# Optimization experiments

Measured on AMD Instinct MI355X. Metric: run time of the kernel, lower is better.

Reference implementation:

```python
import jax, jax.numpy as jnp
import numpy as np

N_NODES = 50000
N_EDGES = 800000
DIM = 256


def setup_inputs() -> dict:
    key = jax.random.key(0)
    k1, k2, k3, k4 = jax.random.split(key, 4)
    x = jax.random.normal(k1, (N_NODES, DIM), dtype=jnp.float32)
    edge_index = jax.random.randint(k2, (2, N_EDGES), 0, N_NODES, dtype=jnp.int64)
    # GCNConv learned params (glorot-style weight, zero bias like PyG default init)
    W = jax.random.normal(k3, (DIM, DIM), dtype=jnp.float32) * (1.0 / np.sqrt(DIM))
    b = jnp.zeros((DIM,), dtype=jnp.float32)
    return {"x": x, "edge_index": edge_index, "W": W, "b": b}


def reference(x, edge_index, W, b):
    # GNNBlock forward (eval mode: dropout is identity; normalizer=Identity,
    # activation=ReLU, projection=Identity since in_dim==out_dim).
    n = x.shape[0]
    # --- GCNConv with self-loops and symmetric normalization ---
    loop = jnp.arange(n, dtype=edge_index.dtype)
    src = jnp.concatenate([edge_index[0], loop])  # [E+N]
    dst = jnp.concatenate([edge_index[1], loop])  # [E+N]
    ones = jnp.ones(src.shape[0], dtype=x.dtype)
    deg = jax.ops.segment_sum(ones, dst, num_segments=n)  # in-degree incl. self-loop
    dinv = jnp.where(deg > 0, jax.lax.rsqrt(deg), 0.0)
    norm = dinv[src] * dinv[dst]  # [E+N]
    h = x @ W  # transform first (in->out), then aggregate
    msg = h[src] * norm[:, None]  # gather + scale, [E+N, DIM]
    agg = jax.ops.segment_sum(msg, dst, num_segments=n) + b  # scatter-add
    # --- norm (Identity) -> activation (ReLU) -> residual -> dropout (eval) ---
    out = jax.nn.relu(agg) + x
    return out
```

## Files before the change

### kernel.cpp

```cpp
#include <hip/hip_runtime.h>

#define N_NODES 50000
#define DIM 256
#define NBUCK 196
#define BCAP 6144
#define CEDGES 2048
#define APAD 264
#define EPAD 260
#define TROWS 32

typedef __attribute__((ext_vector_type(8))) short bf16x8;
typedef __attribute__((ext_vector_type(4))) float f32x4;
typedef __attribute__((ext_vector_type(2))) float f32x2;
union U16 { uint4 u; bf16x8 s; };

__device__ __forceinline__ unsigned short f2b(float f) {
    unsigned int u = __float_as_uint(f);
    return (unsigned short)((u + 0x7FFFu + ((u >> 16) & 1u)) >> 16);
}

__global__ __launch_bounds__(256) void prep_bin_kernel(const int* __restrict__ src,
                                                       const int* __restrict__ dst, int E,
                                                       int nCoarse,
                                                       unsigned int* __restrict__ slab2,
                                                       int* __restrict__ meta,
                                                       const float* __restrict__ W,
                                                       uint4* __restrict__ Bpack,
                                                       const float* __restrict__ x,
                                                       unsigned int* __restrict__ xq) {
    __shared__ int hist[NBUCK];
    __shared__ int scn[NBUCK];
    __shared__ int cur[NBUCK];
    __shared__ int s2[256];
    __shared__ unsigned int sorted[CEDGES];

    const int tid = threadIdx.x;

    if (blockIdx.x >= (unsigned)nCoarse) {
        int role = blockIdx.x - nCoarse;
        if (role < 32) {
            int gid  = role * 256 + tid;
            int lane = gid & 63;
            int u    = (gid >> 6) & 15;
            int ki   = gid >> 10;
            int n    = u * 16 + (lane & 15);
            int k0   = ki * 32 + (lane >> 4) * 8;
            unsigned int w[4];
            #pragma unroll
            for (int p = 0; p < 4; ++p) {
                unsigned int lo = f2b(W[(size_t)(k0 + 2 * p) * DIM + n]);
                unsigned int hi = f2b(W[(size_t)(k0 + 2 * p + 1) * DIM + n]);
                w[p] = lo | (hi << 16);
            }
            Bpack[gid] = make_uint4(w[0], w[1], w[2], w[3]);
        } else {
            int gid = (role - 32) * 256 + tid;
            float4 v = ((const float4*)x)[gid];
            int p = __builtin_amdgcn_cvt_pk_fp8_f32(v.x, v.y, 0, false);
            p     = __builtin_amdgcn_cvt_pk_fp8_f32(v.z, v.w, p, true);
            xq[gid] = (unsigned int)p;
        }
        return;
    }

    const int e0 = blockIdx.x * CEDGES;
    const int nE = min(CEDGES, E - e0);

    if (tid < NBUCK) hist[tid] = 0;
    __syncthreads();

    unsigned int pk[8];
    #pragma unroll
    for (int i = 0; i < 8; ++i) {
        int idx = i * 256 + tid;
        pk[i] = 0xFFFFFFFFu;
        if (idx < nE) {
            unsigned int s = (unsigned int)src[e0 + idx];
            unsigned int d = (unsigned int)dst[e0 + idx];
            pk[i] = (d << 16) | s;
            atomicAdd(&hist[d >> 8], 1);
        }
    }
    __syncthreads();

    int v = (tid < NBUCK) ? hist[tid] : 0;
    s2[tid] = v;
    __syncthreads();
    for (int off = 1; off < 256; off <<= 1) {
        int t = (tid >= off) ? s2[tid - off] : 0;
        __syncthreads();
        s2[tid] += t;
        __syncthreads();
    }
    if (tid < NBUCK) {
        scn[tid] = s2[tid] - v;
        cur[tid] = 0;
    }
    __syncthreads();

    #pragma unroll
    for (int i = 0; i < 8; ++i) {
        if (pk[i] != 0xFFFFFFFFu) {
            int bkt = pk[i] >> 24;
            int p = scn[bkt] + atomicAdd(&cur[bkt], 1);
            sorted[p] = pk[i];
        }
    }
    __syncthreads();

    for (int i = tid; i < nE; i += 256)
        slab2[(size_t)blockIdx.x * CEDGES + i] = sorted[i];
    if (tid < NBUCK)
        meta[blockIdx.x * NBUCK + tid] = (scn[tid] << 16) | (hist[tid] & 0xFFFF);
}

__global__ __launch_bounds__(256) void fine_kernel(int nCoarse,
                                                   const unsigned int* __restrict__ slab2,
                                                   const int* __restrict__ meta,
                                                   int* __restrict__ offs,
                                                   int* __restrict__ deg,
                                                   float* __restrict__ dinv,
                                                   int* __restrict__ csr_src) {
    __shared__ int hist[256];
    __shared__ int scn[256];
    __shared__ unsigned int stage[BCAP];
    __shared__ int lcur;

    const int tid = threadIdx.x;
    const int g = blockIdx.x;

    if (tid == 0) lcur = 0;
    hist[tid] = 0;
    __syncthreads();

    for (int b = tid; b < nCoarse; b += 256) {
        int m = meta[b * NBUCK + g];
        int n  = m & 0xFFFF;
        int st = (m >> 16) & 0xFFFF;
        if (n > 0) {
            int pos = atomicAdd(&lcur, n);
            const unsigned int* rs = slab2 + (size_t)b * CEDGES + st;
            for (int k = 0; k < n; ++k) {
                if (pos + k < BCAP) {
                    unsigned int p = rs[k];
                    stage[pos + k] = p;
                    atomicAdd(&hist[(p >> 16) & 255], 1);
                }
            }
        }
    }
    __syncthreads();
    const int cnt = min(lcur, BCAP);

    int d = hist[tid];
    scn[tid] = d;
    __syncthreads();
    for (int off = 1; off < 256; off <<= 1) {
        int t = (tid >= off) ? scn[tid - off] : 0;
        __syncthreads();
        scn[tid] += t;
        __syncthreads();
    }
    int excl = scn[tid] - d;

    int node = g * 256 + tid;
    const int base = g * BCAP;
    if (node < N_NODES) {
        offs[node] = base + excl;
        deg[node]  = d;
        dinv[node] = rsqrtf((float)(d + 1));
    }
    hist[tid] = excl;
    __syncthreads();

    for (int i = tid; i < cnt; i += 256) {
        unsigned int p = stage[i];
        int pos = atomicAdd(&hist[(p >> 16) & 255], 1);
        csr_src[base + pos] = (int)(p & 0xFFFFu);
    }
}

__global__ __launch_bounds__(256) void agg_gemm_kernel(const unsigned int* __restrict__ xq,
                                                       const int* __restrict__ offs,
                                                       const int* __restrict__ deg,
                                                       const int* __restrict__ csr_src,
                                                       const float* __restrict__ dinv,
                                                       const float* __restrict__ x,
                                                       const uint4* __restrict__ Bpack,
                                                       const float* __restrict__ b,
                                                       float* __restrict__ out) {
    __shared__ __align__(16) char LDSraw[TROWS * EPAD * 4];
    ushort* ALDS = (ushort*)LDSraw;
    float*  ELDS = (float*)LDSraw;

    const int tid  = threadIdx.x;
    const int wave = tid >> 6;
    const int lane = tid & 63;
    const int row0 = blockIdx.x * TROWS;

    for (int j = 0; j < 8; ++j) {
        const int r   = wave * 8 + j;
        const int row = row0 + r;
        ushort4 st4 = make_ushort4(0, 0, 0, 0);
        if (row < N_NODES) {
            const float di = dinv[row];
            unsigned int qself = xq[(size_t)row * 64 + lane];
            f32x2 lo = __builtin_amdgcn_cvt_pk_f32_fp8((int)qself, false);
            f32x2 hi = __builtin_amdgcn_cvt_pk_f32_fp8((int)qself, true);
            float ax = lo.x * di, ay = lo.y * di, az = hi.x * di, aw = hi.y * di;

            const int start = offs[row];
            const int n     = deg[row];
            int i = 0;
            for (; i + 8 <= n; i += 8) {
                int s0 = csr_src[start + i + 0], s1 = csr_src[start + i + 1];
                int s2 = csr_src[start + i + 2], s3 = csr_src[start + i + 3];
                int s4 = csr_src[start + i + 4], s5 = csr_src[start + i + 5];
                int s6 = csr_src[start + i + 6], s7 = csr_src[start + i + 7];
                unsigned int q0 = xq[(size_t)s0 * 64 + lane];
                unsigned int q1 = xq[(size_t)s1 * 64 + lane];
                unsigned int q2 = xq[(size_t)s2 * 64 + lane];
                unsigned int q3 = xq[(size_t)s3 * 64 + lane];
                unsigned int q4 = xq[(size_t)s4 * 64 + lane];
                unsigned int q5 = xq[(size_t)s5 * 64 + lane];
                unsigned int q6 = xq[(size_t)s6 * 64 + lane];
                unsigned int q7 = xq[(size_t)s7 * 64 + lane];
                float d0 = dinv[s0], d1 = dinv[s1], d2 = dinv[s2], d3 = dinv[s3];
                float d4 = dinv[s4], d5 = dinv[s5], d6 = dinv[s6], d7 = dinv[s7];
                #pragma unroll
                for (int u = 0; u < 8; ++u) {
                    unsigned int q; float dd;
                    switch (u) {
                        case 0: q = q0; dd = d0; break; case 1: q = q1; dd = d1; break;
                        case 2: q = q2; dd = d2; break; case 3: q = q3; dd = d3; break;
                        case 4: q = q4; dd = d4; break; case 5: q = q5; dd = d5; break;
                        case 6: q = q6; dd = d6; break; default: q = q7; dd = d7; break;
                    }
                    f32x2 l = __builtin_amdgcn_cvt_pk_f32_fp8((int)q, false);
                    f32x2 h = __builtin_amdgcn_cvt_pk_f32_fp8((int)q, true);
                    ax += l.x * dd; ay += l.y * dd; az += h.x * dd; aw += h.y * dd;
                }
            }
            for (; i < n; ++i) {
                int s = csr_src[start + i];
                unsigned int q = xq[(size_t)s * 64 + lane];
                float dd = dinv[s];
                f32x2 l = __builtin_amdgcn_cvt_pk_f32_fp8((int)q, false);
                f32x2 h = __builtin_amdgcn_cvt_pk_f32_fp8((int)q, true);
                ax += l.x * dd; ay += l.y * dd; az += h.x * dd; aw += h.y * dd;
            }
            ax *= di; ay *= di; az *= di; aw *= di;
            st4 = make_ushort4(f2b(ax), f2b(ay), f2b(az), f2b(aw));
        }
        *(ushort4*)&ALDS[r * APAD + lane * 4] = st4;
    }
    __syncthreads();

    const int m  = lane & 15;
    const int kb = lane >> 4;

    f32x4 acc[2][4];
    #pragma unroll
    for (int r = 0; r < 2; ++r)
        #pragma unroll
        for (int t = 0; t < 4; ++t) acc[r][t] = (f32x4){0.f, 0.f, 0.f, 0.f};

    const uint4* bp = Bpack + (size_t)(wave * 4) * 64 + lane;

    for (int ki = 0; ki < 8; ++ki) {
        U16 bf[4], af[2];
        #pragma unroll
        for (int t = 0; t < 4; ++t) bf[t].u = bp[(size_t)(ki * 16 + t) * 64];
        #pragma unroll
        for (int r = 0; r < 2; ++r)
            af[r].u = *(const uint4*)&ALDS[(r * 16 + m) * APAD + ki * 32 + kb * 8];
        #pragma unroll
        for (int r = 0; r < 2; ++r)
            #pragma unroll
            for (int t = 0; t < 4; ++t)
                acc[r][t] = __builtin_amdgcn_mfma_f32_16x16x32_bf16(af[r].s, bf[t].s, acc[r][t], 0, 0, 0);
    }

    __syncthreads();
    #pragma unroll
    for (int t = 0; t < 4; ++t) {
        #pragma unroll
        for (int rl = 0; rl < 2; ++rl) {
            #pragma unroll
            for (int reg = 0; reg < 4; ++reg) {
                ELDS[(rl * 16 + kb * 4 + reg) * EPAD + wave * 64 + t * 16 + m] = acc[rl][t][reg];
            }
        }
    }
    __syncthreads();

    const float4* x4g = (const float4*)x;
    const float4* b4  = (const float4*)b;
    float4* out4 = (float4*)out;

    #pragma unroll
    for (int j = 0; j < 8; ++j) {
        int idx  = j * 256 + tid;
        int lrow = idx >> 6;
        int c4   = idx & 63;
        int grow = row0 + lrow;
        if (grow < N_NODES) {
            float4 v  = *(const float4*)&ELDS[lrow * EPAD + c4 * 4];
            float4 bb = b4[c4];
            float4 xx = x4g[(size_t)grow * 64 + c4];
            float4 o;
            o.x = fmaxf(v.x + bb.x, 0.f) + xx.x;
            o.y = fmaxf(v.y + bb.y, 0.f) + xx.y;
            o.z = fmaxf(v.z + bb.z, 0.f) + xx.z;
            o.w = fmaxf(v.w + bb.w, 0.f) + xx.w;
            out4[(size_t)grow * 64 + c4] = o;
        }
    }
}

extern "C" void kernel_launch(void* const* d_in, const int* in_sizes, int n_in,
                              void* d_out, int out_size, void* d_ws, size_t ws_size,
                              hipStream_t stream) {
    const float* x  = (const float*)d_in[0];
    const int*   ei = (const int*)d_in[1];
    const float* W  = (const float*)d_in[2];
    const float* b  = (const float*)d_in[3];
    float* out = (float*)d_out;
    const int E = in_sizes[1] / 2;

    char* ws = (char*)d_ws;
    int*          deg     = (int*)(ws);
    int*          offs    = (int*)(ws + 262144);
    float*        dinv    = (float*)(ws + 524288);
    int*          csr_src = (int*)(ws + 786432);
    int*          meta    = (int*)(ws + 5767168);
    unsigned int* slab2   = (unsigned int*)(ws + 6291456);
    uint4*        Bpack   = (uint4*)(ws + 9699328);
    unsigned int* xq      = (unsigned int*)(ws + 10485760);

    const int* src = ei;
    const int* dst = ei + E;

    const int nCoarse = (E + CEDGES - 1) / CEDGES;
    const int nXq = (N_NODES * 64) / 256;

    prep_bin_kernel<<<nCoarse + 32 + nXq, 256, 0, stream>>>(src, dst, E, nCoarse,
                                                            slab2, meta, W, Bpack, x, xq);
    fine_kernel<<<NBUCK, 256, 0, stream>>>(nCoarse, slab2, meta, offs, deg, dinv, csr_src);
    agg_gemm_kernel<<<(N_NODES + TROWS - 1) / TROWS, 256, 0, stream>>>(xq, offs, deg, csr_src,
                                                                       dinv, x, Bpack, b, out);
}
```

Baseline: 208.4 us.

## Parallelize fine-bucket gather via prefix-scanned run map; halve agg-GEMM tile rows

```diff
diff --git a/kernel.cpp b/kernel.cpp
--- a/kernel.cpp
+++ b/kernel.cpp
@@ -7,7 +7,7 @@
 #define CEDGES 2048
 #define APAD 264
 #define EPAD 260
-#define TROWS 32
+#define TROWS 16
 
 typedef __attribute__((ext_vector_type(8))) short bf16x8;
 typedef __attribute__((ext_vector_type(4))) float f32x4;
@@ -121,36 +121,61 @@
                                                    int* __restrict__ deg,
                                                    float* __restrict__ dinv,
                                                    int* __restrict__ csr_src) {
+    __shared__ int rcnt[512];
+    __shared__ int rst[512];
+    __shared__ int rbase[512];
+    __shared__ int scn[256];
     __shared__ int hist[256];
-    __shared__ int scn[256];
+    __shared__ unsigned short rmap[BCAP];
     __shared__ unsigned int stage[BCAP];
-    __shared__ int lcur;
 
     const int tid = threadIdx.x;
     const int g = blockIdx.x;
 
-    if (tid == 0) lcur = 0;
-    hist[tid] = 0;
-    __syncthreads();
-
     for (int b = tid; b < nCoarse; b += 256) {
         int m = meta[b * NBUCK + g];
-        int n  = m & 0xFFFF;
-        int st = (m >> 16) & 0xFFFF;
-        if (n > 0) {
-            int pos = atomicAdd(&lcur, n);
-            const unsigned int* rs = slab2 + (size_t)b * CEDGES + st;
-            for (int k = 0; k < n; ++k) {
-                if (pos + k < BCAP) {
-                    unsigned int p = rs[k];
-                    stage[pos + k] = p;
-                    atomicAdd(&hist[(p >> 16) & 255], 1);
-                }
-            }
-        }
-    }
-    __syncthreads();
-    const int cnt = min(lcur, BCAP);
+        rcnt[b] = m & 0xFFFF;
+        rst[b]  = (m >> 16) & 0xFFFF;
+    }
+    for (int b = nCoarse + tid; b < 512; b += 256) rcnt[b] = 0;
+    __syncthreads();
+
+    int c0 = rcnt[2 * tid];
+    int c1 = rcnt[2 * tid + 1];
+    int ps = c0 + c1;
+    scn[tid] = ps;
+    __syncthreads();
+    for (int off = 1; off < 256; off <<= 1) {
+        int t = (tid >= off) ? scn[tid - off] : 0;
+        __syncthreads();
+        scn[tid] += t;
+        __syncthreads();
+    }
+    int pexcl = scn[tid] - ps;
+    rbase[2 * tid]     = pexcl;
+    rbase[2 * tid + 1] = pexcl + c0;
+    const int total = scn[255];
+    hist[tid] = 0;
+    __syncthreads();
+
+    #pragma unroll
+    for (int rr = 0; rr < 2; ++rr) {
+        int r = 2 * tid + rr;
+        int n = rcnt[r], b0 = rbase[r];
+        for (int k = 0; k < n; ++k)
+            if (b0 + k < BCAP) rmap[b0 + k] = (unsigned short)r;
+    }
+    __syncthreads();
+
+    const int cnt = min(total, BCAP);
+
+    for (int e = tid; e < cnt; e += 256) {
+        int r = rmap[e];
+        unsigned int p = slab2[(size_t)r * CEDGES + rst[r] + (e - rbase[r])];
+        stage[e] = p;
+        atomicAdd(&hist[(p >> 16) & 255], 1);
+    }
+    __syncthreads();
 
     int d = hist[tid];
     scn[tid] = d;
@@ -173,8 +198,8 @@
     hist[tid] = excl;
     __syncthreads();
 
-    for (int i = tid; i < cnt; i += 256) {
-        unsigned int p = stage[i];
+    for (int e = tid; e < cnt; e += 256) {
+        unsigned int p = stage[e];
         int pos = atomicAdd(&hist[(p >> 16) & 255], 1);
         csr_src[base + pos] = (int)(p & 0xFFFFu);
     }
@@ -198,8 +223,8 @@
     const int lane = tid & 63;
     const int row0 = blockIdx.x * TROWS;
 
-    for (int j = 0; j < 8; ++j) {
-        const int r   = wave * 8 + j;
+    for (int j = 0; j < 4; ++j) {
+        const int r   = wave * 4 + j;
         const int row = row0 + r;
         ushort4 st4 = make_ushort4(0, 0, 0, 0);
         if (row < N_NODES) {
@@ -259,37 +284,28 @@
     const int m  = lane & 15;
     const int kb = lane >> 4;
 
-    f32x4 acc[2][4];
-    #pragma unroll
-    for (int r = 0; r < 2; ++r)
-        #pragma unroll
-        for (int t = 0; t < 4; ++t) acc[r][t] = (f32x4){0.f, 0.f, 0.f, 0.f};
+    f32x4 acc[4];
+    #pragma unroll
+    for (int t = 0; t < 4; ++t) acc[t] = (f32x4){0.f, 0.f, 0.f, 0.f};
 
     const uint4* bp = Bpack + (size_t)(wave * 4) * 64 + lane;
 
     for (int ki = 0; ki < 8; ++ki) {
-        U16 bf[4], af[2];
+        U16 bf[4], af;
         #pragma unroll
         for (int t = 0; t < 4; ++t) bf[t].u = bp[(size_t)(ki * 16 + t) * 64];
+        af.u = *(const uint4*)&ALDS[m * APAD + ki * 32 + kb * 8];
         #pragma unroll
-        for (int r = 0; r < 2; ++r)
-            af[r].u = *(const uint4*)&ALDS[(r * 16 + m) * APAD + ki * 32 + kb * 8];
-        #pragma unroll
-        for (int r = 0; r < 2; ++r)
-            #pragma unroll
-            for (int t = 0; t < 4; ++t)
-                acc[r][t] = __builtin_amdgcn_mfma_f32_16x16x32_bf16(af[r].s, bf[t].s, acc[r][t], 0, 0, 0);
+        for (int t = 0; t < 4; ++t)
+            acc[t] = __builtin_amdgcn_mfma_f32_16x16x32_bf16(af.s, bf[t].s, acc[t], 0, 0, 0);
     }
 
     __syncthreads();
     #pragma unroll
     for (int t = 0; t < 4; ++t) {
         #pragma unroll
-        for (int rl = 0; rl < 2; ++rl) {
-            #pragma unroll
-            for (int reg = 0; reg < 4; ++reg) {
-                ELDS[(rl * 16 + kb * 4 + reg) * EPAD + wave * 64 + t * 16 + m] = acc[rl][t][reg];
-            }
+        for (int reg = 0; reg < 4; ++reg) {
+            ELDS[(kb * 4 + reg) * EPAD + wave * 64 + t * 16 + m] = acc[t][reg];
         }
     }
     __syncthreads();
@@ -299,7 +315,7 @@
     float4* out4 = (float4*)out;
 
     #pragma unroll
-    for (int j = 0; j < 8; ++j) {
+    for (int j = 0; j < 4; ++j) {
         int idx  = j * 256 + tid;
         int lrow = idx >> 6;
         int c4   = idx & 63;
```

Result: faster. 190.2 us (-8.7%).
